# Optimization experiments

Hardware: AMD Instinct MI355X
Metric: run time of the kernel (lower is better)

## Reference

```python
import jax, jax.numpy as jnp
import numpy as np
from jax import lax

B, S, D, H = 32, 1024, 1024, 1024


def setup_inputs() -> dict:
    key = jax.random.key(0)
    k_x, k_wx, k_wh, k_b = jax.random.split(key, 4)
    x = jax.random.normal(k_x, (B, S, D), dtype=jnp.float32)
    # Vanilla RNN cell parameters: h' = tanh(x @ Wx + h @ Wh + b)
    Wx = jax.random.normal(k_wx, (D, H), dtype=jnp.float32) / np.sqrt(D)
    Wh = jax.random.normal(k_wh, (H, H), dtype=jnp.float32) / np.sqrt(H)
    b = jnp.zeros((H,), dtype=jnp.float32)
    # initial_hidden weight, zero-initialized as in the keras layer
    h0 = jnp.zeros((H,), dtype=jnp.float32)
    return {"x": x, "Wx": Wx, "Wh": Wh, "b": b, "h0": h0}


def reference(x, Wx, Wh, b, h0):
    # x: [B, S, D] -> scan over time (seq-major, like tf.scan on transposed input)
    batch = x.shape[0]
    h_init = jnp.tile(h0[None, :], (batch, 1))  # [B, H]

    def step(h, x_t):
        h_new = jnp.tanh(x_t @ Wx + h @ Wh + b)  # [B, H]
        return h_new, h_new

    x_sbd = jnp.transpose(x, (1, 0, 2))  # [S, B, D]
    _, out_sbh = lax.scan(step, h_init, x_sbd)
    return jnp.transpose(out_sbh, (1, 0, 2))  # [B, S, H]
```

## Files before the change

### kernel.cpp

```cpp
#include <hip/hip_runtime.h>
#include <hip/hip_bf16.h>


#define BB 32
#define SS 1024
#define DD 1024
#define HH 1024
#define NG 64
#define BG 4
#define WGN (NG * BG)

#define CFENCE() asm volatile("" ::: "memory")

typedef unsigned long long ull;

__global__ __launch_bounds__(256) void xw_gemm(const float* __restrict__ A,
                                               const float* __restrict__ W,
                                               const float* __restrict__ bias,
                                               float* __restrict__ C) {
    __shared__ float As[8][132];
    __shared__ float Bs[8][132];
    const int tid = threadIdx.x;
    const int n0 = blockIdx.x * 128;
    const int m0 = blockIdx.y * 128;
    const int tx = tid & 15;
    const int ty = tid >> 4;
    const int ar = tid >> 1;
    const int ak = (tid & 1) * 4;
    const int bk = tid >> 5;
    const int bn = (tid & 31) * 4;

    float acc[8][8];
#pragma unroll
    for (int i = 0; i < 8; ++i)
#pragma unroll
        for (int j = 0; j < 8; ++j) acc[i][j] = 0.f;

    for (int k0 = 0; k0 < DD; k0 += 8) {
        float4 av = *(const float4*)(A + (size_t)(m0 + ar) * DD + k0 + ak);
        float4 bv = *(const float4*)(W + (size_t)(k0 + bk) * HH + n0 + bn);
        __syncthreads();
        As[ak + 0][ar] = av.x;
        As[ak + 1][ar] = av.y;
        As[ak + 2][ar] = av.z;
        As[ak + 3][ar] = av.w;
        *(float4*)&Bs[bk][bn] = bv;
        __syncthreads();
#pragma unroll
        for (int k = 0; k < 8; ++k) {
            float4 a0 = *(const float4*)&As[k][ty * 4];
            float4 a1 = *(const float4*)&As[k][64 + ty * 4];
            float4 b0 = *(const float4*)&Bs[k][tx * 4];
            float4 b1 = *(const float4*)&Bs[k][64 + tx * 4];
            float ar_[8] = {a0.x, a0.y, a0.z, a0.w, a1.x, a1.y, a1.z, a1.w};
            float br_[8] = {b0.x, b0.y, b0.z, b0.w, b1.x, b1.y, b1.z, b1.w};
#pragma unroll
            for (int i = 0; i < 8; ++i)
#pragma unroll
                for (int j = 0; j < 8; ++j)
                    acc[i][j] = fmaf(ar_[i], br_[j], acc[i][j]);
        }
    }

    float4 bv0 = *(const float4*)(bias + n0 + tx * 4);
    float4 bv1 = *(const float4*)(bias + n0 + 64 + tx * 4);
#pragma unroll
    for (int i = 0; i < 8; ++i) {
        int m = m0 + ((i < 4) ? (ty * 4 + i) : (64 + ty * 4 + (i - 4)));
        float4 r0 = {acc[i][0] + bv0.x, acc[i][1] + bv0.y,
                     acc[i][2] + bv0.z, acc[i][3] + bv0.w};
        float4 r1 = {acc[i][4] + bv1.x, acc[i][5] + bv1.y,
                     acc[i][6] + bv1.z, acc[i][7] + bv1.w};
        *(float4*)(C + (size_t)m * HH + n0 + tx * 4) = r0;
        *(float4*)(C + (size_t)m * HH + n0 + 64 + tx * 4) = r1;
    }
}

__global__ __launch_bounds__(256) void transpose_wh(const float* __restrict__ in,
                                                    float* __restrict__ outT) {
    __shared__ float tile[32][33];
    const int tx = threadIdx.x & 31;
    const int ty = threadIdx.x >> 5;
    const int x0 = blockIdx.x * 32;
    const int y0 = blockIdx.y * 32;
    for (int r = ty; r < 32; r += 8)
        tile[r][tx] = in[(size_t)(y0 + r) * HH + x0 + tx];
    __syncthreads();
    for (int r = ty; r < 32; r += 8)
        outT[(size_t)(x0 + r) * HH + y0 + tx] = tile[tx][r];
}

#define FMA_HALF(HALF)                                                         \
    {                                                                          \
        const int kb = (HALF) * 512 + kq * 4;                                  \
        float4 h[8];                                                           \
        _Pragma("unroll") for (int b = 0; b < 8; ++b)                          \
            h[b] = *(const float4*)&hs[b][kb];                                 \
        _Pragma("unroll") for (int b = 0; b < 8; ++b)                          \
            _Pragma("unroll") for (int c = 0; c < 8; ++c)                      \
                a[b * 8 + c] += h[b].x * wreg[HALF][c].x +                     \
                                h[b].y * wreg[HALF][c].y +                     \
                                h[b].z * wreg[HALF][c].z +                     \
                                h[b].w * wreg[HALF][c].w;                      \
    }

__global__ __launch_bounds__(256, 1) void rnn_persist(
    const float* __restrict__ Wh, const float* __restrict__ WhT,
    const float* __restrict__ h0, float* __restrict__ out,
    unsigned int* __restrict__ flags, float* __restrict__ hbuf) {
    __shared__ float hs[8][1024];
    __shared__ float red[4][64];
    __shared__ float hout[8][16];

    const int tid  = threadIdx.x;
    const int ng   = blockIdx.x & 63;
    const int bg   = blockIdx.x >> 6;
    const int n0   = ng * 16;
    const int b0   = bg * 8;
    const int lane = tid & 63;
    const int wv   = tid >> 6;
    const int ns   = tid >> 7;
    const int kq   = tid & 127;
    unsigned int* cnt = flags + bg * 64;

    float4 wreg[2][8];
    if (WhT) {
        const float* base = WhT + (size_t)(n0 + ns * 8) * HH + kq * 4;
#pragma unroll
        for (int c = 0; c < 8; ++c) {
            wreg[0][c] = *(const float4*)(base + (size_t)c * HH);
            wreg[1][c] = *(const float4*)(base + (size_t)c * HH + 512);
        }
    } else {
#pragma unroll
        for (int c = 0; c < 8; ++c) {
            float v[8];
            for (int j = 0; j < 4; ++j)
                v[j] = Wh[(size_t)(kq * 4 + j) * HH + n0 + ns * 8 + c];
            for (int j = 0; j < 4; ++j)
                v[4 + j] = Wh[(size_t)(512 + kq * 4 + j) * HH + n0 + ns * 8 + c];
            wreg[0][c] = {v[0], v[1], v[2], v[3]};
            wreg[1][c] = {v[4], v[5], v[6], v[7]};
        }
    }

    size_t xp_base = 0;
    int eb = 0, ec = 0;
    if (tid < 128) {
        int l   = tid & 63;
        int idx = (int)(__brev((unsigned)l) >> 26);
        eb = idx >> 3;
        ec = (tid >> 6) * 8 + (idx & 7);
        xp_base = ((size_t)(b0 + eb) * SS) * HH + (n0 + ec);
    }

    for (int t = 0; t < SS; ++t) {
        float xp = 0.f;
        if (tid < 128) xp = out[xp_base + (size_t)t * HH];

        float a[64];
#pragma unroll
        for (int i = 0; i < 64; ++i) a[i] = 0.f;

        if (t == 0) {
#pragma unroll
            for (int j = 0; j < 8; ++j) {
                int f4 = tid + 256 * j;
                int r = f4 >> 8, c4 = (f4 & 255) * 4;
                *(float4*)&hs[r][c4] = *(const float4*)(h0 + c4);
            }
            __syncthreads();
            FMA_HALF(0)
            FMA_HALF(1)
        } else {
            if (tid == 0) {
                const unsigned target = (unsigned)t * 64u;
                while (__hip_atomic_load(cnt, __ATOMIC_RELAXED,
                                         __HIP_MEMORY_SCOPE_AGENT) < target) {
                }
            }
            CFENCE();
            __syncthreads();
            CFENCE();

            const ull* hsrc = (const ull*)(hbuf + (size_t)((t - 1) & 1) * BB * HH);
            ull hr[16];
#pragma unroll
            for (int j = 0; j < 8; ++j)
                hr[j] = __hip_atomic_load(hsrc + (size_t)(b0 + j) * 512 + tid,
                                          __ATOMIC_RELAXED, __HIP_MEMORY_SCOPE_AGENT);
#pragma unroll
            for (int j = 0; j < 8; ++j)
                hr[8 + j] = __hip_atomic_load(hsrc + (size_t)(b0 + j) * 512 + 256 + tid,
                                              __ATOMIC_RELAXED, __HIP_MEMORY_SCOPE_AGENT);
#pragma unroll
            for (int j = 0; j < 8; ++j)
                *(ull*)&hs[j][tid * 2] = hr[j];
            __syncthreads();
            FMA_HALF(0)
#pragma unroll
            for (int j = 0; j < 8; ++j)
                *(ull*)&hs[j][512 + tid * 2] = hr[8 + j];
            __syncthreads();
            FMA_HALF(1)
        }

        int s = 64;
#pragma unroll
        for (int m = 1; m <= 32; m <<= 1) {
            const int hs_ = s >> 1;
            const bool hi = (lane & m) != 0;
#pragma unroll
            for (int i = 0; i < hs_; ++i) {
                float lo = a[i], hg = a[i + hs_];
                a[i]       = hi ? hg : lo;
                a[i + hs_] = hi ? lo : hg;
            }
#pragma unroll
            for (int i = 0; i < hs_; ++i) a[i] += __shfl_xor(a[i + hs_], m, 64);
            s = hs_;
        }

        red[wv][lane] = a[0];
        __syncthreads();

        if (tid < 128) {
            const int l = tid & 63;
            const int nss = tid >> 6;
            float v = red[nss * 2][l] + red[nss * 2 + 1][l];
            float hv = tanhf(v + xp);
            out[xp_base + (size_t)t * HH] = hv;
            hout[eb][ec] = hv;
        }
        __syncthreads();

        if (tid < 64) {
            const int r  = tid >> 3;
            const int c2 = tid & 7;
            ull u = *(const ull*)&hout[r][c2 * 2];
            __hip_atomic_store(
                (ull*)(hbuf + (size_t)(t & 1) * BB * HH) +
                    (size_t)(b0 + r) * 512 + (n0 >> 1) + c2,
                u, __ATOMIC_RELAXED, __HIP_MEMORY_SCOPE_AGENT);
        }

        CFENCE();
        __syncthreads();
        CFENCE();
        if (tid == 0)
            __hip_atomic_fetch_add(cnt, 1u, __ATOMIC_RELAXED,
                                   __HIP_MEMORY_SCOPE_AGENT);
    }
}

__global__ __launch_bounds__(256) void h0wh(const float* __restrict__ Wh,
                                            const float* __restrict__ h0,
                                            float* __restrict__ c) {
    const int g = blockIdx.x;
    const int n = threadIdx.x * 4;
    float4 a = {0.f, 0.f, 0.f, 0.f};
    for (int kk = 0; kk < 16; ++kk) {
        int k = g * 16 + kk;
        float hv = h0[k];
        float4 w = *(const float4*)(Wh + (size_t)k * HH + n);
        a.x += hv * w.x; a.y += hv * w.y; a.z += hv * w.z; a.w += hv * w.w;
    }
    atomicAdd(&c[n + 0], a.x);
    atomicAdd(&c[n + 1], a.y);
    atomicAdd(&c[n + 2], a.z);
    atomicAdd(&c[n + 3], a.w);
}

__global__ __launch_bounds__(256) void t0_kernel(float* __restrict__ out,
                                                 const float* __restrict__ c) {
    const int idx = blockIdx.x * 256 + threadIdx.x;
    const int b = idx >> 10;
    const int n = idx & 1023;
    const size_t p = (size_t)b * SS * HH + n;
    out[p] = tanhf(out[p] + c[n]);
}

__global__ __launch_bounds__(256) void rnn_step(const float* __restrict__ Wh,
                                                float* __restrict__ out, int t) {
    __shared__ float hsl[8][1028];
    __shared__ float ps[256];
    const int tid = threadIdx.x;
    const int n0 = blockIdx.x * 16;
    const int b0 = blockIdx.y * 8;
    for (int i = tid; i < 8 * 256; i += 256) {
        int r = i >> 8;
        int c = (i & 255) << 2;
        *(float4*)&hsl[r][c] =
            *(const float4*)(out + ((size_t)(b0 + r) * SS + (t - 1)) * HH + c);
    }
    __syncthreads();
    const int nl = tid & 15;
    const int bl = (tid >> 4) & 7;
    const int half_ = tid >> 7;
    const int n = n0 + nl;
    float acc = 0.f;
    const float* hrow = &hsl[bl][half_ * 512];
    const float* wcol = Wh + (size_t)(half_ * 512) * HH + n;
#pragma unroll 4
    for (int k = 0; k < 512; k += 4) {
        float4 h4 = *(const float4*)(hrow + k);
        acc += h4.x * wcol[(size_t)(k + 0) * HH];
        acc += h4.y * wcol[(size_t)(k + 1) * HH];
        acc += h4.z * wcol[(size_t)(k + 2) * HH];
        acc += h4.w * wcol[(size_t)(k + 3) * HH];
    }
    ps[tid] = acc;
    __syncthreads();
    if (tid < 128) {
        const size_t obase = ((size_t)(b0 + bl) * SS + t) * HH + n;
        out[obase] = tanhf(out[obase] + ps[tid] + ps[tid + 128]);
    }
}

extern "C" void kernel_launch(void* const* d_in, const int* in_sizes, int n_in,
                              void* d_out, int out_size, void* d_ws, size_t ws_size,
                              hipStream_t stream) {
    const float* x    = (const float*)d_in[0];
    const float* Wx   = (const float*)d_in[1];
    const float* Wh   = (const float*)d_in[2];
    const float* bias = (const float*)d_in[3];
    const float* h0   = (const float*)d_in[4];
    float* out = (float*)d_out;
    float* ws  = (float*)d_ws;

    xw_gemm<<<dim3(8, 256), 256, 0, stream>>>(x, Wx, bias, out);

    const size_t need_persist = (size_t)(256 + 2 * BB * HH) * sizeof(float);
    const size_t need_wht     = need_persist + (size_t)HH * HH * sizeof(float);

    if (ws_size >= need_persist) {
        unsigned int* flags = (unsigned int*)ws;
        float* hbuf = ws + 256;
        hipMemsetAsync(flags, 0, 1024, stream);

        const float* WhT = nullptr;
        if (ws_size >= need_wht) {
            float* whtp = ws + 256 + 2 * BB * HH;
            transpose_wh<<<dim3(32, 32), 256, 0, stream>>>(Wh, whtp);
            WhT = whtp;
        }

        void* kargs[] = {(void*)&Wh, (void*)&WhT, (void*)&h0, (void*)&out,
                         (void*)&flags, (void*)&hbuf};
        hipError_t rc = hipLaunchCooperativeKernel((const void*)rnn_persist,
                                                   dim3(WGN), dim3(256), kargs, 0,
                                                   stream);
        if (rc != hipSuccess) {
            rnn_persist<<<dim3(WGN), dim3(256), 0, stream>>>(Wh, WhT, h0, out,
                                                             flags, hbuf);
        }
    } else {
        float* cvec = ws;
        hipMemsetAsync(cvec, 0, HH * sizeof(float), stream);
        h0wh<<<64, 256, 0, stream>>>(Wh, h0, cvec);
        t0_kernel<<<BB * HH / 256, 256, 0, stream>>>(out, cvec);
        for (int t = 1; t < SS; ++t)
            rnn_step<<<dim3(64, 4), 256, 0, stream>>>(Wh, out, t);
    }
}
```

Baseline: 5.093 ms.

## Replace counter barrier with per-element step-tagged hidden-state handoff

```diff
diff --git a/kernel.cpp b/kernel.cpp
--- a/kernel.cpp
+++ b/kernel.cpp
@@ -10,9 +10,9 @@
 #define BG 4
 #define WGN (NG * BG)
 
-#define CFENCE() asm volatile("" ::: "memory")
-
 typedef unsigned long long ull;
+
+#define ALD(p) __hip_atomic_load((p), __ATOMIC_RELAXED, __HIP_MEMORY_SCOPE_AGENT)
 
 __global__ __launch_bounds__(256) void xw_gemm(const float* __restrict__ A,
                                                const float* __restrict__ W,
@@ -107,7 +107,7 @@
 __global__ __launch_bounds__(256, 1) void rnn_persist(
     const float* __restrict__ Wh, const float* __restrict__ WhT,
     const float* __restrict__ h0, float* __restrict__ out,
-    unsigned int* __restrict__ flags, float* __restrict__ hbuf) {
+    ull* __restrict__ hbuf) {
     __shared__ float hs[8][1024];
     __shared__ float red[4][64];
     __shared__ float hout[8][16];
@@ -121,7 +121,6 @@
     const int wv   = tid >> 6;
     const int ns   = tid >> 7;
     const int kq   = tid & 127;
-    unsigned int* cnt = flags + bg * 64;
 
     float4 wreg[2][8];
     if (WhT) {
@@ -173,34 +172,37 @@
             FMA_HALF(0)
             FMA_HALF(1)
         } else {
-            if (tid == 0) {
-                const unsigned target = (unsigned)t * 64u;
-                while (__hip_atomic_load(cnt, __ATOMIC_RELAXED,
-                                         __HIP_MEMORY_SCOPE_AGENT) < target) {
-                }
-            }
-            CFENCE();
-            __syncthreads();
-            CFENCE();
-
-            const ull* hsrc = (const ull*)(hbuf + (size_t)((t - 1) & 1) * BB * HH);
-            ull hr[16];
-#pragma unroll
-            for (int j = 0; j < 8; ++j)
-                hr[j] = __hip_atomic_load(hsrc + (size_t)(b0 + j) * 512 + tid,
-                                          __ATOMIC_RELAXED, __HIP_MEMORY_SCOPE_AGENT);
-#pragma unroll
-            for (int j = 0; j < 8; ++j)
-                hr[8 + j] = __hip_atomic_load(hsrc + (size_t)(b0 + j) * 512 + 256 + tid,
-                                              __ATOMIC_RELAXED, __HIP_MEMORY_SCOPE_AGENT);
-#pragma unroll
-            for (int j = 0; j < 8; ++j)
-                *(ull*)&hs[j][tid * 2] = hr[j];
+            const ull* hsrc = hbuf + (size_t)((t - 1) & 1) * BB * HH;
+            const unsigned wtag = (unsigned)(t - 1);
+            const ull* rp[8];
+            ull v0[8][2], v1[8][2];
+#pragma unroll
+            for (int r = 0; r < 8; ++r) {
+                const ull* rowp = hsrc + (size_t)(b0 + r) * HH + tid * 2;
+                rp[r] = rowp;
+                v0[r][0] = ALD(rowp);
+                v0[r][1] = ALD(rowp + 1);
+                v1[r][0] = ALD(rowp + 512);
+                v1[r][1] = ALD(rowp + 513);
+            }
+#pragma unroll
+            for (int r = 0; r < 8; ++r) {
+                while ((unsigned)(v0[r][0] >> 32) != wtag) v0[r][0] = ALD(rp[r]);
+                while ((unsigned)(v0[r][1] >> 32) != wtag) v0[r][1] = ALD(rp[r] + 1);
+                float2 f = {__uint_as_float((unsigned)v0[r][0]),
+                            __uint_as_float((unsigned)v0[r][1])};
+                *(float2*)&hs[r][tid * 2] = f;
+            }
             __syncthreads();
             FMA_HALF(0)
 #pragma unroll
-            for (int j = 0; j < 8; ++j)
-                *(ull*)&hs[j][512 + tid * 2] = hr[8 + j];
+            for (int r = 0; r < 8; ++r) {
+                while ((unsigned)(v1[r][0] >> 32) != wtag) v1[r][0] = ALD(rp[r] + 512);
+                while ((unsigned)(v1[r][1] >> 32) != wtag) v1[r][1] = ALD(rp[r] + 513);
+                float2 f = {__uint_as_float((unsigned)v1[r][0]),
+                            __uint_as_float((unsigned)v1[r][1])};
+                *(float2*)&hs[r][512 + tid * 2] = f;
+            }
             __syncthreads();
             FMA_HALF(1)
         }
@@ -234,22 +236,14 @@
         }
         __syncthreads();
 
-        if (tid < 64) {
-            const int r  = tid >> 3;
-            const int c2 = tid & 7;
-            ull u = *(const ull*)&hout[r][c2 * 2];
+        if (tid < 128) {
+            const int r = tid >> 4;
+            const int c = tid & 15;
+            ull u = ((ull)(unsigned)t << 32) | __float_as_uint(hout[r][c]);
             __hip_atomic_store(
-                (ull*)(hbuf + (size_t)(t & 1) * BB * HH) +
-                    (size_t)(b0 + r) * 512 + (n0 >> 1) + c2,
+                hbuf + (size_t)(t & 1) * BB * HH + (size_t)(b0 + r) * HH + n0 + c,
                 u, __ATOMIC_RELAXED, __HIP_MEMORY_SCOPE_AGENT);
         }
-
-        CFENCE();
-        __syncthreads();
-        CFENCE();
-        if (tid == 0)
-            __hip_atomic_fetch_add(cnt, 1u, __ATOMIC_RELAXED,
-                                   __HIP_MEMORY_SCOPE_AGENT);
     }
 }
 
@@ -330,29 +324,27 @@
 
     xw_gemm<<<dim3(8, 256), 256, 0, stream>>>(x, Wx, bias, out);
 
-    const size_t need_persist = (size_t)(256 + 2 * BB * HH) * sizeof(float);
+    const size_t need_persist = (size_t)2 * BB * HH * sizeof(ull);
     const size_t need_wht     = need_persist + (size_t)HH * HH * sizeof(float);
 
     if (ws_size >= need_persist) {
-        unsigned int* flags = (unsigned int*)ws;
-        float* hbuf = ws + 256;
-        hipMemsetAsync(flags, 0, 1024, stream);
+        ull* hbuf = (ull*)ws;
 
         const float* WhT = nullptr;
         if (ws_size >= need_wht) {
-            float* whtp = ws + 256 + 2 * BB * HH;
+            float* whtp = ws + 4 * BB * HH;
             transpose_wh<<<dim3(32, 32), 256, 0, stream>>>(Wh, whtp);
             WhT = whtp;
         }
 
         void* kargs[] = {(void*)&Wh, (void*)&WhT, (void*)&h0, (void*)&out,
-                         (void*)&flags, (void*)&hbuf};
+                         (void*)&hbuf};
         hipError_t rc = hipLaunchCooperativeKernel((const void*)rnn_persist,
                                                    dim3(WGN), dim3(256), kargs, 0,
                                                    stream);
         if (rc != hipSuccess) {
             rnn_persist<<<dim3(WGN), dim3(256), 0, stream>>>(Wh, WhT, h0, out,
-                                                             flags, hbuf);
+                                                             hbuf);
         }
     } else {
         float* cvec = ws;
```

Result: slower. 11.10 ms (+118.0%).
